# Kernel tuning notes

Hardware: AMD Instinct MI355X
Metric: run time of the kernel (lower is better)

The kernel has to match this reference:

```python
import jax, jax.numpy as jnp
import numpy as np

B, N, E = 2, 20000, 320000
ND, ED, HD, L = 64, 32, 256, 4


def setup_inputs() -> dict:
    key = jax.random.key(0)
    ks = jax.random.split(key, 16)
    w = lambda k, shape: jax.random.normal(k, shape, jnp.float32) / np.sqrt(shape[-2])
    return {
        "node_features": jax.random.normal(ks[0], (B, N, ND), jnp.float32),
        "edge_indices": jax.random.randint(ks[1], (B, E, 2), 0, N, jnp.int64),
        "edge_features": jax.random.normal(ks[2], (B, E, ED), jnp.float32),
        "in_W": w(ks[3], (ND, HD)),
        "in_b": jnp.zeros((HD,), jnp.float32),
        "mW1": w(ks[4], (L, 2 * HD + ED, HD)),
        "mb1": jnp.zeros((L, HD), jnp.float32),
        "mW2": w(ks[5], (L, HD, HD)),
        "mb2": jnp.zeros((L, HD), jnp.float32),
        "uW1": w(ks[6], (L, HD + HD, HD)),
        "ub1": jnp.zeros((L, HD), jnp.float32),
        "uW2": w(ks[7], (L, HD, HD)),
        "ub2": jnp.zeros((L, HD), jnp.float32),
        "out_W": w(ks[8], (HD, ND)),
        "out_b": jnp.zeros((ND,), jnp.float32),
    }


def _mp_layer(h, edge_indices, edge_features, W1, b1, W2, b2, V1, c1, V2, c2):
    """One message passing layer, vmapped over batch of graphs."""
    def per_graph(nodes, edges, efeat):
        src = nodes[edges[:, 0]]                      # [E, HD] gather
        dst = nodes[edges[:, 1]]                      # [E, HD] gather
        msg_in = jnp.concatenate([src, dst, efeat], axis=-1)  # [E, 2HD+ED]
        msg = jax.nn.gelu(msg_in @ W1 + b1) @ W2 + b2          # [E, HD]
        agg = jnp.zeros((nodes.shape[0], W2.shape[1]), nodes.dtype)
        agg = agg.at[edges[:, 1]].add(msg)                     # scatter-add [N, HD]
        upd_in = jnp.concatenate([nodes, agg], axis=-1)        # [N, 2HD]
        return jax.nn.gelu(upd_in @ V1 + c1) @ V2 + c2         # [N, HD]

    return jax.vmap(per_graph)(h, edge_indices, edge_features)


def reference(node_features, edge_indices, edge_features, in_W, in_b,
              mW1, mb1, mW2, mb2, uW1, ub1, uW2, ub2, out_W, out_b):
    h = node_features @ in_W + in_b                  # [B, N, HD]
    num_layers = mW1.shape[0]
    for l in range(num_layers):
        h_new = _mp_layer(h, edge_indices, edge_features,
                          mW1[l], mb1[l], mW2[l], mb2[l],
                          uW1[l], ub1[l], uW2[l], ub2[l])
        h = h + h_new                                # residual
    return h @ out_W + out_b                         # [B, N, ND]
```

## Files before the change

### kernel.cpp

```cpp
#include <hip/hip_runtime.h>

#define NN 20000
#define NE 320000
#define NB 2
#define HDIM 256
#define NDIM 64
#define EDIM 32
#define NL 4

typedef short short8 __attribute__((ext_vector_type(8)));
typedef float f32x4 __attribute__((ext_vector_type(4)));

__device__ __forceinline__ float gelu_af(float x) {
    float x3 = x * x * x;
    float e = exp2f(2.3022082f * fmaf(0.044715f, x3, x));
    return fmaf(-x, __builtin_amdgcn_rcpf(e + 1.0f), x);
}

__device__ __forceinline__ unsigned short f2bf(float f) {
    unsigned int x = __float_as_uint(f);
    unsigned int r = (x + 0x7fffu + ((x >> 16) & 1u)) >> 16;
    return (unsigned short)r;
}
__device__ __forceinline__ float bf2f(unsigned short h) {
    return __uint_as_float(((unsigned int)h) << 16);
}

__global__ __launch_bounds__(256) void tr_k(
    const float* __restrict__ inW, const float* __restrict__ mW1,
    const float* __restrict__ mW2, const float* __restrict__ uW1,
    const float* __restrict__ uW2, const float* __restrict__ outW,
    unsigned short* __restrict__ dst)
{
    const int id = blockIdx.z;
    const float* src; int K, N; size_t doff;
    if (id == 0)       { src = inW;  K = 64;  N = 256; doff = 0; }
    else if (id <= 4)  { int l = id - 1;  src = mW1 + (size_t)l * 544 * 256; K = 544; N = 256; doff = 16384   + (size_t)l * 139264; }
    else if (id <= 8)  { int l = id - 5;  src = mW2 + (size_t)l * 256 * 256; K = 256; N = 256; doff = 573440  + (size_t)l * 65536;  }
    else if (id <= 12) { int l = id - 9;  src = uW1 + (size_t)l * 512 * 256; K = 512; N = 256; doff = 835584  + (size_t)l * 131072; }
    else if (id <= 16) { int l = id - 13; src = uW2 + (size_t)l * 256 * 256; K = 256; N = 256; doff = 1359872 + (size_t)l * 65536;  }
    else               { src = outW; K = 256; N = 64;  doff = 1622016; }

    const int k0 = blockIdx.x * 32, n0 = blockIdx.y * 32;
    if (k0 >= K || n0 >= N) return;

    __shared__ float tile[32][33];
    const int tx = threadIdx.x & 31, ty = threadIdx.x >> 5;
    #pragma unroll
    for (int i = 0; i < 4; ++i) {
        int k = k0 + ty + i * 8, n = n0 + tx;
        tile[ty + i * 8][tx] = (k < K && n < N) ? src[(size_t)k * N + n] : 0.f;
    }
    __syncthreads();
    #pragma unroll
    for (int i = 0; i < 4; ++i) {
        int n = n0 + ty + i * 8, k = k0 + tx;
        if (n < N && k < K) dst[doff + (size_t)n * K + k] = f2bf(tile[tx][ty + i * 8]);
    }
}

__global__ __launch_bounds__(256) void wv_k(
    const float* __restrict__ mW2, const float* __restrict__ uW1,
    unsigned short* __restrict__ w2v1bT)
{
    const int l = blockIdx.z;
    const float* W2  = mW2 + (size_t)l * 65536;
    const float* V1b = uW1 + (size_t)l * 131072 + 65536;
    const int n0 = blockIdx.x * 16, k0 = blockIdx.y * 16;
    const int tx = threadIdx.x & 15, ty = threadIdx.x >> 4;
    __shared__ float sW[16][17], sV[16][17];
    float acc = 0.f;
    for (int j0 = 0; j0 < 256; j0 += 16) {
        sW[ty][tx] = W2[(size_t)(k0 + ty) * 256 + j0 + tx];
        sV[ty][tx] = V1b[(size_t)(j0 + ty) * 256 + n0 + tx];
        __syncthreads();
        #pragma unroll
        for (int jj = 0; jj < 16; ++jj)
            acc = fmaf(sW[ty][jj], sV[jj][tx], acc);
        __syncthreads();
    }
    w2v1bT[(size_t)l * 65536 + (size_t)(n0 + tx) * 256 + (k0 + ty)] = f2bf(acc);
}

__global__ void bv_k(const float* __restrict__ mb1, const float* __restrict__ mb2,
                     const float* __restrict__ uW1,
                     float* __restrict__ b2v, float* __restrict__ bias512)
{
    const int l = blockIdx.x, t = threadIdx.x;
    if (t < 256) {
        const float* V1b = uW1 + (size_t)l * 131072 + 65536;
        const float* b2  = mb2 + l * 256;
        float s = 0.f;
        for (int j = 0; j < 256; ++j) s = fmaf(b2[j], V1b[(size_t)j * 256 + t], s);
        b2v[l * 256 + t] = s;
    }
    bias512[l * 512 + t] = (t < 256) ? 0.f : mb1[l * 256 + (t - 256)];
}

template <int MODE, int ASPLIT, int CSPLIT>
__global__ __launch_bounds__(256) void mgemm_k(
    const float* __restrict__ A,
    const unsigned short* __restrict__ Ah, const unsigned short* __restrict__ Al,
    const unsigned short* __restrict__ BT, int ldb,
    const unsigned short* __restrict__ A2h, const unsigned short* __restrict__ A2l,
    const unsigned short* __restrict__ BT2, int ldb2,
    const float* __restrict__ bias, const float* __restrict__ bias2,
    const float* __restrict__ degf,
    float* __restrict__ C, unsigned short* __restrict__ Ch, unsigned short* __restrict__ Cl,
    int M, int N, int K, int K2, int bkoff)
{
    __shared__ unsigned char smem[64 * 80 * 2 + 128 * 80];
    unsigned char* ahi = smem;
    unsigned char* alo = smem + 64 * 80;
    unsigned char* btl = smem + 64 * 80 * 2;

    const int tid = threadIdx.x;
    const int bm = blockIdx.x * 64;
    const int bn = blockIdx.y * 128;
    const int w = tid >> 6, lane = tid & 63;
    const int wr = w >> 1, wc = w & 1;
    const int lrow = lane & 15, lg = lane >> 4;

    f32x4 acc[2][4];
    #pragma unroll
    for (int i = 0; i < 2; ++i)
        #pragma unroll
        for (int j = 0; j < 4; ++j) acc[i][j] = (f32x4){0.f, 0.f, 0.f, 0.f};

    const int t1 = K >> 5, t2 = K2 >> 5;
    for (int t = 0; t < t1 + t2; ++t) {
        int k0, lda, ldbv;
        const float* Ap; const unsigned short* Ahp; const unsigned short* Alp;
        const unsigned short* Bp;
        if (t < t1) { Ap = A;  Ahp = Ah;  Alp = Al;  Bp = BT;  k0 = t * 32;        lda = K;  ldbv = ldb;  }
        else        { Ap = nullptr; Ahp = A2h; Alp = A2l; Bp = BT2; k0 = (t - t1) * 32; lda = K2; ldbv = ldb2; }

        {
            const int row = tid >> 2, kq = (tid & 3) * 8;
            const int m = bm + row;
            if (ASPLIT) {
                uint4 hv = make_uint4(0u, 0u, 0u, 0u), lv = hv;
                if (m < M) {
                    hv = *(const uint4*)&Ahp[(size_t)m * lda + k0 + kq];
                    lv = *(const uint4*)&Alp[(size_t)m * lda + k0 + kq];
                }
                *(uint4*)(ahi + row * 80 + kq * 2) = hv;
                *(uint4*)(alo + row * 80 + kq * 2) = lv;
            } else {
                float4 v0 = make_float4(0.f, 0.f, 0.f, 0.f), v1 = v0;
                if (m < M) {
                    v0 = *(const float4*)&Ap[(size_t)m * lda + k0 + kq];
                    v1 = *(const float4*)&Ap[(size_t)m * lda + k0 + kq + 4];
                }
                float vv[8] = {v0.x, v0.y, v0.z, v0.w, v1.x, v1.y, v1.z, v1.w};
                unsigned short hh[8], ll[8];
                #pragma unroll
                for (int j = 0; j < 8; ++j) {
                    hh[j] = f2bf(vv[j]);
                    ll[j] = f2bf(vv[j] - bf2f(hh[j]));
                }
                ushort4 ph0 = {hh[0], hh[1], hh[2], hh[3]}, ph1 = {hh[4], hh[5], hh[6], hh[7]};
                ushort4 pl0 = {ll[0], ll[1], ll[2], ll[3]}, pl1 = {ll[4], ll[5], ll[6], ll[7]};
                *(ushort4*)(ahi + row * 80 + kq * 2)     = ph0;
                *(ushort4*)(ahi + row * 80 + kq * 2 + 8) = ph1;
                *(ushort4*)(alo + row * 80 + kq * 2)     = pl0;
                *(ushort4*)(alo + row * 80 + kq * 2 + 8) = pl1;
            }
        }
        {
            const int row = tid >> 1, half = tid & 1;
            const int n = bn + row;
            const unsigned short* brow = Bp + (size_t)(n & 255) * ldbv + (n >> 8) * bkoff;
            #pragma unroll
            for (int c = 0; c < 2; ++c) {
                const int q = half * 2 + c;
                uint4 d = make_uint4(0u, 0u, 0u, 0u);
                if (n < N) d = *(const uint4*)&brow[k0 + q * 8];
                *(uint4*)(btl + row * 80 + q * 16) = d;
            }
        }
        __syncthreads();

        short8 ah[2], al[2], bfr[4];
        #pragma unroll
        for (int mi = 0; mi < 2; ++mi) {
            const int r = wr * 32 + mi * 16 + lrow;
            ah[mi] = *(const short8*)(ahi + r * 80 + lg * 16);
            al[mi] = *(const short8*)(alo + r * 80 + lg * 16);
        }
        #pragma unroll
        for (int ni = 0; ni < 4; ++ni) {
            const int r = wc * 64 + ni * 16 + lrow;
            bfr[ni] = *(const short8*)(btl + r * 80 + lg * 16);
        }
        #pragma unroll
        for (int mi = 0; mi < 2; ++mi)
            #pragma unroll
            for (int ni = 0; ni < 4; ++ni) {
                acc[mi][ni] = __builtin_amdgcn_mfma_f32_16x16x32_bf16(ah[mi], bfr[ni], acc[mi][ni], 0, 0, 0);
                acc[mi][ni] = __builtin_amdgcn_mfma_f32_16x16x32_bf16(al[mi], bfr[ni], acc[mi][ni], 0, 0, 0);
            }
        __syncthreads();
    }

    #pragma unroll
    for (int mi = 0; mi < 2; ++mi) {
        #pragma unroll
        for (int ni = 0; ni < 4; ++ni) {
            const int ncol = bn + wc * 64 + ni * 16 + lrow;
            if (ncol >= N) continue;
            const float bv = bias ? bias[ncol] : 0.f;
            const float b2vv = (MODE == 4) ? bias2[ncol] : 0.f;
            const int mbase = bm + wr * 32 + mi * 16 + lg * 4;
            #pragma unroll
            for (int r = 0; r < 4; ++r) {
                const int m = mbase + r;
                if (m >= M) continue;
                const size_t cb = (size_t)m * N + ncol;
                float v = acc[mi][ni][r];
                if (MODE == 0)      v += bv;
                else if (MODE == 3) v += bf2f(Ch[cb]) + bf2f(Cl[cb]) + bv;
                else                v = gelu_af(v + degf[m] * b2vv + bv);
                if (CSPLIT) {
                    unsigned short hi = f2bf(v);
                    unsigned short lo = f2bf(v - bf2f(hi));
                    Ch[cb] = hi; Cl[cb] = lo;
                } else {
                    C[cb] = v;
                }
            }
        }
    }
}

__global__ void hist2_k(const int* __restrict__ ei, int* __restrict__ cnt) {
    int i = blockIdx.x * blockDim.x + threadIdx.x;
    if (i < NB * NE) {
        const int g = i / NE, e = i - g * NE;
        atomicAdd(&cnt[g * NN + ei[(size_t)g * NE * 2 + 2 * e + 1]], 1);
    }
}

__global__ void scan2_k(const int* __restrict__ cnt_all, int* __restrict__ row_ptr_all,
                        int* __restrict__ cursor_all, float* __restrict__ degf_all) {
    const int g = blockIdx.x;
    const int* cnt = cnt_all + g * NN;
    int* row_ptr = row_ptr_all + g * (NN + 1);
    int* cursor  = cursor_all + g * NN;
    float* degf  = degf_all + g * NN;
    __shared__ int part[256];
    int tid = threadIdx.x;
    const int per = (NN + 255) >> 8;
    int s0 = tid * per;
    int s1 = s0 + per; if (s1 > NN) s1 = NN; if (s0 > NN) s0 = NN;
    int sum = 0;
    for (int i = s0; i < s1; ++i) sum += cnt[i];
    part[tid] = sum;
    __syncthreads();
    if (tid == 0) {
        int r = 0;
        for (int i = 0; i < 256; ++i) { int v = part[i]; part[i] = r; r += v; }
    }
    __syncthreads();
    int off = part[tid];
    for (int i = s0; i < s1; ++i) {
        int c = cnt[i];
        row_ptr[i] = off; cursor[i] = off; degf[i] = (float)c;
        off += c;
    }
    if (tid == 255) row_ptr[NN] = off;
}

__global__ void fill2_k(const int* __restrict__ ei, int* __restrict__ cursor,
                        int* __restrict__ csr_src, int* __restrict__ csr_eid) {
    int i = blockIdx.x * blockDim.x + threadIdx.x;
    if (i < NB * NE) {
        const int g = i / NE, e = i - g * NE;
        const int* eig = ei + (size_t)g * NE * 2;
        int s = eig[2 * e + 0];
        int d = eig[2 * e + 1];
        int pos = atomicAdd(&cursor[g * NN + d], 1);
        csr_src[(size_t)g * NE + pos] = s;
        csr_eid[(size_t)g * NE + pos] = e;
    }
}

__global__ __launch_bounds__(256, 4) void edge_agg5_k(
    const float* __restrict__ T12, const float* __restrict__ efeat,
    const unsigned short* __restrict__ w1t,
    const int* __restrict__ csr_src, const int* __restrict__ csr_eid,
    const int* __restrict__ row_ptr,
    unsigned short* __restrict__ Shi, unsigned short* __restrict__ Slo)
{
    __shared__ unsigned short efo[4][16 * 260];

    const int tid = threadIdx.x;
    const int g   = blockIdx.x / (NN / 4);
    const int blk = blockIdx.x % (NN / 4);
    const int wave = tid >> 6, lane = tid & 63;
    const int lrow = lane & 15, lg = lane >> 4;
    const int d = blk * 4 + wave;

    const float* T12g = T12 + (size_t)g * NN * 512;
    const float* efg  = efeat + (size_t)g * NE * EDIM;
    const int* csG    = csr_src + (size_t)g * NE;
    const int* ceG    = csr_eid + (size_t)g * NE;
    const int* rpG    = row_ptr + (size_t)g * (NN + 1);

    const int dstart = rpG[d], dend = rpG[d + 1];
    const int c0 = lane * 4;

    short8 bfrag[16];
    #pragma unroll
    for (int ni = 0; ni < 16; ++ni)
        bfrag[ni] = *(const short8*)&w1t[(size_t)(ni * 16 + lrow) * 544 + 512 + lg * 8];

    const float4 hd = *(const float4*)&T12g[(size_t)d * 512 + 256 + c0];
    float4 acc = make_float4(0.f, 0.f, 0.f, 0.f);
    unsigned short* efw = &efo[wave][0];

    for (int P = dstart; P < dend; P += 16) {
        const int nv = dend - P < 16 ? dend - P : 16;
        int pos = P + lrow; if (pos >= dend) pos = dend - 1;

        const int eid  = ceG[pos];
        const int myid = csG[pos];

        const float* er = &efg[(size_t)eid * EDIM + lg * 8];
        float4 v0 = *(const float4*)er;
        float4 v1 = *(const float4*)(er + 4);
        short8 af;
        af[0] = (short)f2bf(v0.x); af[1] = (short)f2bf(v0.y);
        af[2] = (short)f2bf(v0.z); af[3] = (short)f2bf(v0.w);
        af[4] = (short)f2bf(v1.x); af[5] = (short)f2bf(v1.y);
        af[6] = (short)f2bf(v1.z); af[7] = (short)f2bf(v1.w);

        #pragma unroll
        for (int ni = 0; ni < 16; ++ni) {
            f32x4 a4 = (f32x4){0.f, 0.f, 0.f, 0.f};
            a4 = __builtin_amdgcn_mfma_f32_16x16x32_bf16(af, bfrag[ni], a4, 0, 0, 0);
            #pragma unroll
            for (int r = 0; r < 4; ++r)
                efw[(4 * lg + r) * 260 + ni * 16 + lrow] = f2bf(a4[r]);
        }

        for (int p = P; p < P + nv; p += 4) {
            const int nc = P + nv - p;
            int sj[4]; float4 hs[4]; ushort4 ef4[4];
            #pragma unroll
            for (int j = 0; j < 4; ++j) {
                const int q = p + ((j < nc) ? j : 0);
                sj[j] = __shfl(myid, q - P, 64);
            }
            #pragma unroll
            for (int j = 0; j < 4; ++j) {
                const int q = p + ((j < nc) ? j : 0);
                hs[j] = *(const float4*)&T12g[(size_t)sj[j] * 512 + c0];
                ef4[j] = *(const ushort4*)&efw[(q - P) * 260 + c0];
            }
            #pragma unroll
            for (int j = 0; j < 4; ++j) {
                if (j < nc) {
                    acc.x += gelu_af(hs[j].x + hd.x + bf2f(ef4[j].x));
                    acc.y += gelu_af(hs[j].y + hd.y + bf2f(ef4[j].y));
                    acc.z += gelu_af(hs[j].z + hd.z + bf2f(ef4[j].z));
                    acc.w += gelu_af(hs[j].w + hd.w + bf2f(ef4[j].w));
                }
            }
        }
    }

    ushort4 ho, lo;
    ho.x = f2bf(acc.x); lo.x = f2bf(acc.x - bf2f(ho.x));
    ho.y = f2bf(acc.y); lo.y = f2bf(acc.y - bf2f(ho.y));
    ho.z = f2bf(acc.z); lo.z = f2bf(acc.z - bf2f(ho.z));
    ho.w = f2bf(acc.w); lo.w = f2bf(acc.w - bf2f(ho.w));
    *(ushort4*)&Shi[((size_t)g * NN + d) * HDIM + c0] = ho;
    *(ushort4*)&Slo[((size_t)g * NN + d) * HDIM + c0] = lo;
}

extern "C" void kernel_launch(void* const* d_in, const int* in_sizes, int n_in,
                              void* d_out, int out_size, void* d_ws, size_t ws_size,
                              hipStream_t stream)
{
    const float* nf    = (const float*)d_in[0];
    const int*   ei    = (const int*)  d_in[1];
    const float* efeat = (const float*)d_in[2];
    const float* inW   = (const float*)d_in[3];
    const float* inb   = (const float*)d_in[4];
    const float* mW1   = (const float*)d_in[5];
    const float* mb1   = (const float*)d_in[6];
    const float* mW2   = (const float*)d_in[7];
    const float* mb2   = (const float*)d_in[8];
    const float* uW1   = (const float*)d_in[9];
    const float* ub1   = (const float*)d_in[10];
    const float* uW2   = (const float*)d_in[11];
    const float* ub2   = (const float*)d_in[12];
    const float* outW  = (const float*)d_in[13];
    const float* outb  = (const float*)d_in[14];
    float* outp = (float*)d_out;

    const int MT = NB * NN;

    char* p = (char*)d_ws;
    auto carve = [&](size_t bytes) -> void* {
        void* r = (void*)p;
        p += (bytes + 255) & ~(size_t)255;
        return r;
    };
    unsigned short* hS  = (unsigned short*)carve((size_t)2 * MT * HDIM * 2);
    unsigned short* T3S = (unsigned short*)carve((size_t)2 * MT * HDIM * 2);
    float* T12 = (float*)carve((size_t)MT * 512 * 4);
    unsigned short* US = (unsigned short*)T12;
    int* csr_src = (int*)carve((size_t)NB * NE * 4);
    int* csr_eid = (int*)carve((size_t)NB * NE * 4);
    int* row_ptr = (int*)carve((size_t)NB * (NN + 1) * 4);
    int* cursor  = (int*)carve((size_t)NB * NN * 4);
    int* cnt     = (int*)carve((size_t)NB * NN * 4);
    float* degf  = (float*)carve((size_t)MT * 4);
    unsigned short* wtbuf  = (unsigned short*)carve((size_t)1638400 * 2);
    unsigned short* w2v1bT = (unsigned short*)carve((size_t)4 * 65536 * 2);
    float* b2v     = (float*)carve((size_t)4 * 256 * 4);
    float* bias512 = (float*)carve((size_t)4 * 512 * 4);
    (void)ws_size; (void)in_sizes; (void)n_in; (void)out_size;

    unsigned short* hHi  = hS;   unsigned short* hLo  = hS  + (size_t)MT * HDIM;
    unsigned short* t3Hi = T3S;  unsigned short* t3Lo = T3S + (size_t)MT * HDIM;
    unsigned short* uHi  = US;   unsigned short* uLo  = US  + (size_t)MT * HDIM;

    const dim3 blk(256);
    const dim3 gIn(625, 2), gHsHd(625, 4), gU(625, 2), gRes(625, 2), gOut(625, 1);
    const dim3 gE(NB * NN / 4);

    tr_k<<<dim3(17, 8, 18), blk, 0, stream>>>(inW, mW1, mW2, uW1, uW2, outW, wtbuf);
    wv_k<<<dim3(16, 16, 4), blk, 0, stream>>>(mW2, uW1, w2v1bT);
    bv_k<<<dim3(4), dim3(512), 0, stream>>>(mb1, mb2, uW1, b2v, bias512);

    const unsigned short* wtIn  = wtbuf;
    const unsigned short* wtW1  = wtbuf + 16384;
    const unsigned short* wtU1  = wtbuf + 835584;
    const unsigned short* wtU2  = wtbuf + 1359872;
    const unsigned short* wtOut = wtbuf + 1622016;

    hipMemsetAsync(cnt, 0, (size_t)NB * NN * sizeof(int), stream);
    hist2_k<<<(NB * NE + 255) / 256, blk, 0, stream>>>(ei, cnt);
    scan2_k<<<dim3(NB), blk, 0, stream>>>(cnt, row_ptr, cursor, degf);
    fill2_k<<<(NB * NE + 255) / 256, blk, 0, stream>>>(ei, cursor, csr_src, csr_eid);

    mgemm_k<0, 0, 1><<<gIn, blk, 0, stream>>>(
        nf, nullptr, nullptr, wtIn, NDIM,
        nullptr, nullptr, nullptr, 0,
        inb, nullptr, nullptr,
        nullptr, hHi, hLo, MT, HDIM, NDIM, 0, 0);

    for (int l = 0; l < NL; ++l) {
        const unsigned short* w1t = wtW1 + (size_t)l * 139264;
        const unsigned short* u1t = wtU1 + (size_t)l * 131072;
        const unsigned short* u2t = wtU2 + (size_t)l * 65536;

        mgemm_k<0, 1, 0><<<gHsHd, blk, 0, stream>>>(
            nullptr, hHi, hLo, w1t, 544,
            nullptr, nullptr, nullptr, 0,
            bias512 + l * 512, nullptr, nullptr,
            T12, nullptr, nullptr, MT, 512, HDIM, 0, 256);

        edge_agg5_k<<<gE, blk, 0, stream>>>(T12, efeat, w1t,
                                            csr_src, csr_eid, row_ptr,
                                            t3Hi, t3Lo);

        mgemm_k<4, 1, 1><<<gU, blk, 0, stream>>>(
            nullptr, hHi, hLo, u1t, 512,
            t3Hi, t3Lo, w2v1bT + (size_t)l * 65536, 256,
            ub1 + l * HDIM, b2v + l * 256, degf,
            nullptr, uHi, uLo, MT, HDIM, HDIM, HDIM, 0);

        mgemm_k<3, 1, 1><<<gRes, blk, 0, stream>>>(
            nullptr, uHi, uLo, u2t, HDIM,
            nullptr, nullptr, nullptr, 0,
            ub2 + l * HDIM, nullptr, nullptr,
            nullptr, hHi, hLo, MT, HDIM, HDIM, 0, 0);
    }

    mgemm_k<0, 1, 0><<<gOut, blk, 0, stream>>>(
        nullptr, hHi, hLo, wtOut, HDIM,
        nullptr, nullptr, nullptr, 0,
        outb, nullptr, nullptr,
        outp, nullptr, nullptr, MT, NDIM, HDIM, 0, 0);
}
```

Before: 1.328 ms.

## Pack CSR src/eid pairs, shrink edge chunk to 8, raise occupancy

Packs the CSR source and edge-id arrays into one int2 array so each edge needs a single 8-byte load. Cuts the per-wave edge chunk from 16 to 8, which halves the LDS staging buffer, and raises launch bounds from 4 to 8 waves per SIMD to hide gather latency. Also uses 32-bit byte offsets for the T12 gathers. The MFMA still computes 16 rows, so half of that work is now wasted, and register pressure from the 16 bfrag fragments may cause spills at the higher occupancy.

```diff
diff --git a/kernel.cpp b/kernel.cpp
--- a/kernel.cpp
+++ b/kernel.cpp
@@ -7,6 +7,7 @@
 #define NDIM 64
 #define EDIM 32
 #define NL 4
+#define CHUNK 8
 
 typedef short short8 __attribute__((ext_vector_type(8)));
 typedef float f32x4 __attribute__((ext_vector_type(4)));
@@ -272,7 +273,7 @@
 }
 
 __global__ void fill2_k(const int* __restrict__ ei, int* __restrict__ cursor,
-                        int* __restrict__ csr_src, int* __restrict__ csr_eid) {
+                        int2* __restrict__ csr_pack) {
     int i = blockIdx.x * blockDim.x + threadIdx.x;
     if (i < NB * NE) {
         const int g = i / NE, e = i - g * NE;
@@ -280,19 +281,17 @@
         int s = eig[2 * e + 0];
         int d = eig[2 * e + 1];
         int pos = atomicAdd(&cursor[g * NN + d], 1);
-        csr_src[(size_t)g * NE + pos] = s;
-        csr_eid[(size_t)g * NE + pos] = e;
-    }
-}
-
-__global__ __launch_bounds__(256, 4) void edge_agg5_k(
+        csr_pack[(size_t)g * NE + pos] = make_int2(s, e);
+    }
+}
+
+__global__ __launch_bounds__(256, 8) void edge_agg6_k(
     const float* __restrict__ T12, const float* __restrict__ efeat,
     const unsigned short* __restrict__ w1t,
-    const int* __restrict__ csr_src, const int* __restrict__ csr_eid,
-    const int* __restrict__ row_ptr,
+    const int2* __restrict__ csr_pack, const int* __restrict__ row_ptr,
     unsigned short* __restrict__ Shi, unsigned short* __restrict__ Slo)
 {
-    __shared__ unsigned short efo[4][16 * 260];
+    __shared__ unsigned short efo[4][CHUNK * 260];
 
     const int tid = threadIdx.x;
     const int g   = blockIdx.x / (NN / 4);
@@ -303,28 +302,28 @@
 
     const float* T12g = T12 + (size_t)g * NN * 512;
     const float* efg  = efeat + (size_t)g * NE * EDIM;
-    const int* csG    = csr_src + (size_t)g * NE;
-    const int* ceG    = csr_eid + (size_t)g * NE;
+    const int2* cpG   = csr_pack + (size_t)g * NE;
     const int* rpG    = row_ptr + (size_t)g * (NN + 1);
 
     const int dstart = rpG[d], dend = rpG[d + 1];
     const int c0 = lane * 4;
+    const char* tb = (const char*)T12g;
 
     short8 bfrag[16];
     #pragma unroll
     for (int ni = 0; ni < 16; ++ni)
         bfrag[ni] = *(const short8*)&w1t[(size_t)(ni * 16 + lrow) * 544 + 512 + lg * 8];
 
-    const float4 hd = *(const float4*)&T12g[(size_t)d * 512 + 256 + c0];
+    const float4 hd = *(const float4*)(tb + (unsigned)d * 2048u + 1024u + (unsigned)c0 * 4u);
     float4 acc = make_float4(0.f, 0.f, 0.f, 0.f);
     unsigned short* efw = &efo[wave][0];
 
-    for (int P = dstart; P < dend; P += 16) {
-        const int nv = dend - P < 16 ? dend - P : 16;
-        int pos = P + lrow; if (pos >= dend) pos = dend - 1;
-
-        const int eid  = ceG[pos];
-        const int myid = csG[pos];
+    for (int P = dstart; P < dend; P += CHUNK) {
+        const int nv = dend - P < CHUNK ? dend - P : CHUNK;
+        int pos = P + (lrow & 7); if (pos >= dend) pos = dend - 1;
+
+        const int2 cp = cpG[pos];
+        const int myid = cp.x, eid = cp.y;
 
         const float* er = &efg[(size_t)eid * EDIM + lg * 8];
         float4 v0 = *(const float4*)er;
@@ -339,9 +338,11 @@
         for (int ni = 0; ni < 16; ++ni) {
             f32x4 a4 = (f32x4){0.f, 0.f, 0.f, 0.f};
             a4 = __builtin_amdgcn_mfma_f32_16x16x32_bf16(af, bfrag[ni], a4, 0, 0, 0);
-            #pragma unroll
-            for (int r = 0; r < 4; ++r)
-                efw[(4 * lg + r) * 260 + ni * 16 + lrow] = f2bf(a4[r]);
+            if (lg < 2) {
+                #pragma unroll
+                for (int r = 0; r < 4; ++r)
+                    efw[(4 * lg + r) * 260 + ni * 16 + lrow] = f2bf(a4[r]);
+            }
         }
 
         for (int p = P; p < P + nv; p += 4) {
@@ -355,7 +356,7 @@
             #pragma unroll
             for (int j = 0; j < 4; ++j) {
                 const int q = p + ((j < nc) ? j : 0);
-                hs[j] = *(const float4*)&T12g[(size_t)sj[j] * 512 + c0];
+                hs[j] = *(const float4*)(tb + (unsigned)sj[j] * 2048u + (unsigned)c0 * 4u);
                 ef4[j] = *(const ushort4*)&efw[(q - P) * 260 + c0];
             }
             #pragma unroll
@@ -412,8 +413,7 @@
     unsigned short* T3S = (unsigned short*)carve((size_t)2 * MT * HDIM * 2);
     float* T12 = (float*)carve((size_t)MT * 512 * 4);
     unsigned short* US = (unsigned short*)T12;
-    int* csr_src = (int*)carve((size_t)NB * NE * 4);
-    int* csr_eid = (int*)carve((size_t)NB * NE * 4);
+    int2* csr_pack = (int2*)carve((size_t)NB * NE * 8);
     int* row_ptr = (int*)carve((size_t)NB * (NN + 1) * 4);
     int* cursor  = (int*)carve((size_t)NB * NN * 4);
     int* cnt     = (int*)carve((size_t)NB * NN * 4);
@@ -445,7 +445,7 @@
     hipMemsetAsync(cnt, 0, (size_t)NB * NN * sizeof(int), stream);
     hist2_k<<<(NB * NE + 255) / 256, blk, 0, stream>>>(ei, cnt);
     scan2_k<<<dim3(NB), blk, 0, stream>>>(cnt, row_ptr, cursor, degf);
-    fill2_k<<<(NB * NE + 255) / 256, blk, 0, stream>>>(ei, cursor, csr_src, csr_eid);
+    fill2_k<<<(NB * NE + 255) / 256, blk, 0, stream>>>(ei, cursor, csr_pack);
 
     mgemm_k<0, 0, 1><<<gIn, blk, 0, stream>>>(
         nf, nullptr, nullptr, wtIn, NDIM,
@@ -464,8 +464,8 @@
             bias512 + l * 512, nullptr, nullptr,
             T12, nullptr, nullptr, MT, 512, HDIM, 0, 256);
 
-        edge_agg5_k<<<gE, blk, 0, stream>>>(T12, efeat, w1t,
-                                            csr_src, csr_eid, row_ptr,
+        edge_agg6_k<<<gE, blk, 0, stream>>>(T12, efeat, w1t,
+                                            csr_pack, row_ptr,
                                             t3Hi, t3Lo);
 
         mgemm_k<4, 1, 1><<<gU, blk, 0, stream>>>(
```

Measured after the change: 2.428 ms. 82.8% more time.
